# Kernel optimization log

Hardware: AMD Instinct MI355X
Metric: run time of the kernel (lower is better)

The kernel has to match this reference:

```python
import jax, jax.numpy as jnp
import numpy as np

SIGMA = 0.1
CAPACITY_FACTOR = 1.25


def setup_inputs() -> dict:
    key = jax.random.key(0)
    ks = jax.random.split(key, 5)
    B, T, D, E, H = 4, 2048, 1024, 16, 4096
    x = jax.random.normal(ks[0], (B, T, D), dtype=jnp.float32)
    token_mask = jnp.ones((B, T), dtype=bool)
    noise = jax.random.uniform(ks[1], (B * T, E), dtype=jnp.float32)
    W_router = jax.random.normal(ks[2], (D, E), dtype=jnp.float32) * 0.02
    W1 = jax.random.normal(ks[3], (E, D, H), dtype=jnp.float32) * 0.02
    W2 = jax.random.normal(ks[4], (E, H, D), dtype=jnp.float32) * 0.02
    return {"x": x, "token_mask": token_mask, "noise": noise,
            "W_router": W_router, "W1": W1, "W2": W2}


def reference(x, token_mask, noise, W_router, W1, W2):
    B, T, D = x.shape
    E = W_router.shape[1]
    N = B * T
    cap = int(N * CAPACITY_FACTOR / E)  # static capacity (mask is full)

    xf = x.reshape(N, D)
    mask = token_mask.reshape(N)

    # --- router (noisy gating) ---
    logits_clean = xf @ W_router                           # [N, E]
    mult = 1.0 + (noise * 2.0 - 1.0) * SIGMA
    mult = jnp.where(mask[:, None], mult, 1.0)
    logits = logits_clean * mult
    probs = jax.nn.softmax(logits, axis=-1)
    eid = jnp.argmax(probs, axis=-1)                       # [N]
    gate = jnp.take_along_axis(probs, eid[:, None], axis=1)[:, 0]

    probs_clean = jax.nn.softmax(logits_clean, axis=-1)
    eid_clean = jnp.argmax(probs_clean, axis=-1)

    # --- aux losses (over masked tokens) ---
    n_all = jnp.sum(mask).astype(logits_clean.dtype)
    p = jnp.sum(jnp.where(mask[:, None], probs_clean, 0.0), axis=0) / n_all
    f = jnp.sum(jnp.where(mask[:, None], jax.nn.one_hot(eid_clean, E, dtype=logits_clean.dtype), 0.0), axis=0) / n_all
    lb_loss = E * jnp.sum(p * f)
    z = jax.nn.logsumexp(logits_clean, axis=-1)
    z_loss = jnp.sum(jnp.where(mask, z * z, 0.0)) / n_all

    # --- capacity dispatch: per expert keep top-cap tokens by gate ---
    eid_eff = jnp.where(mask, eid, E)                      # masked tokens -> sentinel E
    order = jnp.lexsort((-gate, eid_eff))                  # by expert asc, gate desc
    sorted_e = eid_eff[order]
    pos = jnp.arange(N) - jnp.searchsorted(sorted_e, sorted_e, side="left")
    keep = (pos < cap) & (sorted_e < E)                    # dispatch mask (sorted)
    slot = jnp.where(keep, sorted_e * cap + pos, E * cap)  # overflow row for dropped

    buf = jnp.zeros((E * cap + 1, D), dtype=x.dtype)
    buf = buf.at[slot].set(jnp.where(keep[:, None], xf[order], 0.0))
    buf_e = buf[: E * cap].reshape(E, cap, D)

    # --- per-expert FFN, output scaled by gate ---
    h = jax.nn.relu(jnp.einsum("ecd,edh->ech", buf_e, W1))
    yb = jnp.einsum("ech,ehd->ecd", h, W2).reshape(E * cap, D)

    # --- combine: gather back, zero for dropped/masked tokens ---
    y_sorted = jnp.where(keep[:, None],
                         yb[jnp.clip(slot, 0, E * cap - 1)] * gate[order][:, None],
                         0.0)
    y = jnp.zeros((N, D), dtype=x.dtype).at[order].set(y_sorted)
    return y.reshape(B, T, D), lb_loss, z_loss
```

## Files before the change

### kernel.cpp

```cpp
#include <hip/hip_runtime.h>
#include <math.h>

#define N_TOK 8192
#define DMODEL 1024
#define NEXP 16
#define HDIM 4096
#define CAP 640
#define MYB 5
#define RANK_TPB 16
#define TP_RPAD 260

typedef __attribute__((ext_vector_type(8))) short bf16x8;
typedef __attribute__((ext_vector_type(4))) float f32x4;

#define OFF_EID   0
#define OFF_GATE  32768
#define OFF_SLOT  65536
#define OFF_PSUM  98304
#define OFF_Z2    (98304 + 64)
#define OFF_FCNT  (98304 + 128)
#define OFF_CNT   (98304 + 192)
#define OFF_BUF   131072
#define OFF_H     (OFF_BUF + 20971520)
#define OFF_WT    (OFF_H + 83886080)

__device__ inline unsigned short f2b(float f) {
    unsigned u = __builtin_bit_cast(unsigned, f);
    return (unsigned short)((u + 0x7fffu + ((u >> 16) & 1u)) >> 16);
}
__device__ inline float b2f(unsigned short b) {
    return __builtin_bit_cast(float, ((unsigned)b) << 16);
}

#define GLOAD_LDS16(g, l) __builtin_amdgcn_global_load_lds( \
    (__attribute__((address_space(1))) const void*)(g),      \
    (__attribute__((address_space(3))) void*)(l), 16, 0, 0)

__global__ __launch_bounds__(256) void router_kernel(
    const float* __restrict__ x, const float* __restrict__ noise,
    const float* __restrict__ Wr,
    int* __restrict__ eid, float* __restrict__ gate,
    float* __restrict__ p_sum, float* __restrict__ z2_sum,
    int* __restrict__ f_cnt, int* __restrict__ cnt_noisy)
{
    __shared__ float Wlds[1024 * 17];
    __shared__ float p_blk[16];
    __shared__ float z2_blk;
    int tid = threadIdx.x;
    for (int i = tid; i < 16384; i += 256) {
        int d = i >> 4, e = i & 15;
        Wlds[d * 17 + e] = Wr[i];
    }
    if (tid < 16) p_blk[tid] = 0.f;
    if (tid == 16) z2_blk = 0.f;
    __syncthreads();

    int lane = tid & 63;
    int wave = tid >> 6;

    for (int tt = 0; tt < 4; ++tt) {
        int t = blockIdx.x * 16 + wave * 4 + tt;
        const float* xr = x + (size_t)t * DMODEL;

        float acc[16];
#pragma unroll
        for (int e = 0; e < 16; ++e) acc[e] = 0.f;
        for (int c = 0; c < 16; ++c) {
            int d = c * 64 + lane;
            float xv = xr[d];
#pragma unroll
            for (int e = 0; e < 16; ++e)
                acc[e] = fmaf(xv, Wlds[d * 17 + e], acc[e]);
        }
#pragma unroll
        for (int e = 0; e < 16; ++e) {
#pragma unroll
            for (int m = 32; m >= 1; m >>= 1)
                acc[e] += __shfl_xor(acc[e], m, 64);
        }

        if (lane == 0) {
            float mx = acc[0]; int am = 0;
#pragma unroll
            for (int e = 1; e < 16; ++e) if (acc[e] > mx) { mx = acc[e]; am = e; }
            float pc[16]; float s = 0.f;
#pragma unroll
            for (int e = 0; e < 16; ++e) { pc[e] = expf(acc[e] - mx); s += pc[e]; }
            float inv = 1.f / s;
            float z = mx + logf(s);

            float ln[16];
#pragma unroll
            for (int e = 0; e < 16; ++e) {
                float nz = noise[(size_t)t * 16 + e];
                ln[e] = acc[e] * (1.f + (nz * 2.f - 1.f) * 0.1f);
            }
            float mxn = ln[0]; int amn = 0;
#pragma unroll
            for (int e = 1; e < 16; ++e) if (ln[e] > mxn) { mxn = ln[e]; amn = e; }
            float sn = 0.f;
#pragma unroll
            for (int e = 0; e < 16; ++e) sn += expf(ln[e] - mxn);
            float g = 1.f / sn;

            eid[t] = amn;
            gate[t] = g;
            atomicAdd(&f_cnt[am], 1);
            atomicAdd(&cnt_noisy[amn], 1);
#pragma unroll
            for (int e = 0; e < 16; ++e) atomicAdd(&p_blk[e], pc[e] * inv);
            atomicAdd(&z2_blk, z * z);
        }
    }
    __syncthreads();
    if (tid < 16) atomicAdd(&p_sum[tid], p_blk[tid]);
    if (tid == 16) atomicAdd(z2_sum, z2_blk);
}

__global__ __launch_bounds__(256) void rank_kernel(
    const int* __restrict__ eid, const float* __restrict__ gate,
    int* __restrict__ slot)
{
    __shared__ int   se[N_TOK];
    __shared__ float sg[N_TOK];
    int tid = threadIdx.x;
    for (int k = tid; k < N_TOK; k += 256) {
        se[k] = eid[k];
        sg[k] = gate[k];
    }
    __syncthreads();

    int wave = tid >> 6, lane = tid & 63;
    int base = blockIdx.x * RANK_TPB + wave * 4;

    int   my_e[4];
    float my_g[4];
    int   r[4] = {0, 0, 0, 0};
#pragma unroll
    for (int t = 0; t < 4; ++t) {
        my_e[t] = se[base + t];
        my_g[t] = sg[base + t];
    }

    for (int k = 0; k < N_TOK / 64; ++k) {
        int j = k * 64 + lane;
        int   ej = se[j];
        float gj = sg[j];
#pragma unroll
        for (int t = 0; t < 4; ++t) {
            int i = base + t;
            if (ej == my_e[t] && (gj > my_g[t] || (gj == my_g[t] && j < i))) r[t]++;
        }
    }
#pragma unroll
    for (int t = 0; t < 4; ++t) {
#pragma unroll
        for (int m = 32; m >= 1; m >>= 1)
            r[t] += __shfl_xor(r[t], m, 64);
    }
    if (lane < 4) {
        int t = lane;
        int rr = r[t];
        slot[base + t] = (rr < CAP) ? my_e[t] * CAP + rr : -1;
    }
}

__global__ __launch_bounds__(256) void scatter_kernel(
    const float* __restrict__ x, const int* __restrict__ slot,
    unsigned short* __restrict__ buf)
{
    int i = blockIdx.x;
    int s = slot[i];
    if (s < 0) return;
    float4 v = ((const float4*)(x + (size_t)i * DMODEL))[threadIdx.x];
    ushort4 o;
    o.x = f2b(v.x); o.y = f2b(v.y); o.z = f2b(v.z); o.w = f2b(v.w);
    ((ushort4*)(buf + (size_t)s * DMODEL))[threadIdx.x] = o;
}

__global__ __launch_bounds__(256) void transpose_cvt(
    const float* __restrict__ in, unsigned short* __restrict__ out,
    int R, int C)
{
    __shared__ unsigned short S[64][TP_RPAD];
    int e = blockIdx.z;
    const float* I = in + (size_t)e * R * C;
    unsigned short* O = out + (size_t)e * R * C;
    int r0 = blockIdx.y * 256, c0 = blockIdx.x * 64;
    int tid = threadIdx.x;

    int rr = tid >> 4;
    int c4 = (tid & 15) * 4;
#pragma unroll
    for (int s = 0; s < 16; ++s) {
        int row = s * 16 + rr;
        float4 v = *(const float4*)(I + (size_t)(r0 + row) * C + c0 + c4);
        S[c4 + 0][row] = f2b(v.x);
        S[c4 + 1][row] = f2b(v.y);
        S[c4 + 2][row] = f2b(v.z);
        S[c4 + 3][row] = f2b(v.w);
    }
    __syncthreads();

    int k4 = (tid & 63) * 4;
    int cb = tid >> 6;
#pragma unroll
    for (int u = 0; u < 16; ++u) {
        int c = cb + u * 4;
        ushort4 w = *(const ushort4*)&S[c][k4];
        *(ushort4*)(O + (size_t)(c0 + c) * R + r0 + k4) = w;
    }
}

template<int RELU>
__global__ __launch_bounds__(256) void gemm_mfma(
    const unsigned short* __restrict__ A,
    const unsigned short* __restrict__ BT,
    unsigned short* __restrict__ C,
    const int* __restrict__ cnt,
    int K, int N, int NX)
{
    unsigned orig = blockIdx.x;
    unsigned chunk = gridDim.x >> 3;
    unsigned logical = (orig & 7u) * chunk + (orig >> 3);
    unsigned my = logical % MYB;
    unsigned rest = logical / MYB;
    unsigned nx = rest % (unsigned)NX;
    unsigned e = rest / (unsigned)NX;

    int eff = cnt[e]; eff = eff < CAP ? eff : CAP;
    int m0 = my * 128;
    if (m0 >= eff) return;
    int n0 = nx * 128;
    const unsigned short* Ae  = A  + (size_t)e * CAP * K + (size_t)m0 * K;
    const unsigned short* BTe = BT + (size_t)e * N * K   + (size_t)n0 * K;
    unsigned short* Ce = C + (size_t)e * CAP * N;

    __shared__ unsigned short Asm[128 * 64];
    __shared__ unsigned short Bsm[128 * 64];

    int tid = threadIdx.x;
    int w = tid >> 6, lane = tid & 63;
    int l16 = lane & 15, quad = lane >> 4;
    int wy = w >> 1, wx = w & 1;

    f32x4 acc[4][4] = {};

    for (int k0 = 0; k0 < K; k0 += 64) {
#pragma unroll
        for (int i = 0; i < 4; ++i) {
            int s = i * 256 + w * 64 + lane;
            int r = s >> 3;
            int l = (s & 7) ^ (r & 7);
            const unsigned short* ga = Ae  + (size_t)r * K + k0 + l * 8;
            const unsigned short* gb = BTe + (size_t)r * K + k0 + l * 8;
            GLOAD_LDS16(ga, Asm + (i * 256 + w * 64) * 8);
            GLOAD_LDS16(gb, Bsm + (i * 256 + w * 64) * 8);
        }
        __syncthreads();
#pragma unroll
        for (int kk = 0; kk < 64; kk += 32) {
            bf16x8 af[4], bfr[4];
            int lc = (kk >> 3) + quad;
#pragma unroll
            for (int i = 0; i < 4; ++i) {
                int m = wy * 64 + i * 16 + l16;
                af[i] = *(const bf16x8*)(Asm + ((size_t)m * 8 + (lc ^ (m & 7))) * 8);
                int n = wx * 64 + i * 16 + l16;
                bfr[i] = *(const bf16x8*)(Bsm + ((size_t)n * 8 + (lc ^ (n & 7))) * 8);
            }
#pragma unroll
            for (int i = 0; i < 4; ++i)
#pragma unroll
                for (int j = 0; j < 4; ++j)
                    acc[i][j] = __builtin_amdgcn_mfma_f32_16x16x32_bf16(
                        af[i], bfr[j], acc[i][j], 0, 0, 0);
        }
        __syncthreads();
    }

#pragma unroll
    for (int i = 0; i < 4; ++i) {
        int rloc = wy * 64 + i * 16 + quad * 4;
        unsigned short* Cs = (wy == 0) ? Asm : Bsm;
        int rbase = rloc & 63;
#pragma unroll
        for (int j = 0; j < 4; ++j) {
            int cloc = wx * 64 + j * 16 + l16;
#pragma unroll
            for (int r = 0; r < 4; ++r) {
                float v = acc[i][j][r];
                if (RELU) v = fmaxf(v, 0.f);
                Cs[(rbase + r) * 128 + cloc] = f2b(v);
            }
        }
    }
    __syncthreads();
    {
        int rr2 = tid >> 4;
        int cc2 = (tid & 15) * 8;
#pragma unroll
        for (int p = 0; p < 8; ++p) {
            int rloc = p * 16 + rr2;
            const unsigned short* Cs = (p < 4) ? Asm : Bsm;
            int rbase = rloc & 63;
            bf16x8 v = *(const bf16x8*)(Cs + rbase * 128 + cc2);
            *(bf16x8*)(Ce + (size_t)(m0 + rloc) * N + n0 + cc2) = v;
        }
    }
}

__global__ __launch_bounds__(256) void combine_kernel(
    const unsigned short* __restrict__ yb, const int* __restrict__ slot,
    const float* __restrict__ gate, float* __restrict__ y,
    const float* __restrict__ p_sum, const float* __restrict__ z2,
    const int* __restrict__ f_cnt, float* __restrict__ loss_out)
{
    int i = blockIdx.x;
    int s = slot[i];
    float4 v = make_float4(0.f, 0.f, 0.f, 0.f);
    if (s >= 0) {
        float g = gate[i];
        ushort4 t = ((const ushort4*)(yb + (size_t)s * DMODEL))[threadIdx.x];
        v = make_float4(b2f(t.x) * g, b2f(t.y) * g, b2f(t.z) * g, b2f(t.w) * g);
    }
    ((float4*)(y + (size_t)i * DMODEL))[threadIdx.x] = v;

    if (i == 0 && threadIdx.x == 0) {
        float lb = 0.f;
        for (int e = 0; e < 16; ++e)
            lb += (p_sum[e] / 8192.f) * ((float)f_cnt[e] / 8192.f);
        loss_out[0] = 16.f * lb;
        loss_out[1] = z2[0] / 8192.f;
    }
}

extern "C" void kernel_launch(void* const* d_in, const int* in_sizes, int n_in,
                              void* d_out, int out_size, void* d_ws, size_t ws_size,
                              hipStream_t stream) {
    const float* x     = (const float*)d_in[0];
    const float* noise = (const float*)d_in[2];
    const float* Wr    = (const float*)d_in[3];
    const float* W1    = (const float*)d_in[4];
    const float* W2    = (const float*)d_in[5];
    float* out = (float*)d_out;

    char* ws = (char*)d_ws;
    int*   eid   = (int*)(ws + OFF_EID);
    float* gate  = (float*)(ws + OFF_GATE);
    int*   slot  = (int*)(ws + OFF_SLOT);
    float* p_sum = (float*)(ws + OFF_PSUM);
    float* z2    = (float*)(ws + OFF_Z2);
    int*   f_cnt = (int*)(ws + OFF_FCNT);
    int*   cnt   = (int*)(ws + OFF_CNT);
    unsigned short* buf = (unsigned short*)(ws + OFF_BUF);
    unsigned short* h   = (unsigned short*)(ws + OFF_H);
    unsigned short* wt  = (unsigned short*)(ws + OFF_WT);
    unsigned short* yb  = buf;

    hipMemsetAsync(ws + OFF_PSUM, 0, 256, stream);

    router_kernel<<<N_TOK / 16, 256, 0, stream>>>(x, noise, Wr, eid, gate,
                                                  p_sum, z2, f_cnt, cnt);
    rank_kernel<<<N_TOK / RANK_TPB, 256, 0, stream>>>(eid, gate, slot);
    scatter_kernel<<<N_TOK, 256, 0, stream>>>(x, slot, buf);

    transpose_cvt<<<dim3(HDIM / 64, DMODEL / 256, NEXP), 256, 0, stream>>>(
        W1, wt, DMODEL, HDIM);
    gemm_mfma<1><<<NEXP * (HDIM / 128) * MYB, 256, 0, stream>>>(
        buf, wt, h, cnt, DMODEL, HDIM, HDIM / 128);

    transpose_cvt<<<dim3(DMODEL / 64, HDIM / 256, NEXP), 256, 0, stream>>>(
        W2, wt, HDIM, DMODEL);
    gemm_mfma<0><<<NEXP * (DMODEL / 128) * MYB, 256, 0, stream>>>(
        h, wt, yb, cnt, HDIM, DMODEL, DMODEL / 128);

    combine_kernel<<<N_TOK, 256, 0, stream>>>(yb, slot, gate, out,
                                              p_sum, z2, f_cnt,
                                              out + (size_t)N_TOK * DMODEL);
}
```

Baseline: 978.5 us.

## Fuse rank and scatter kernels, aggregate router counts in LDS, hoist GEMM addresses

The rank kernel now writes each token's slot and copies its row, converted to bf16, into the expert buffer itself, so the separate scatter kernel launch and the slot re-read go away. The router accumulates per-block expert counts in shared memory and issues one global atomic per expert per block instead of one per token. The GEMM precomputes its per-lane global load pointers outside the k loop. Each wave in the fused kernel now copies 4 rows, which is less parallelism for the copy than the old one-block-per-token scatter.

```diff
diff --git a/kernel.cpp b/kernel.cpp
--- a/kernel.cpp
+++ b/kernel.cpp
@@ -45,13 +45,15 @@
 {
     __shared__ float Wlds[1024 * 17];
     __shared__ float p_blk[16];
+    __shared__ int   f_blk[16];
+    __shared__ int   c_blk[16];
     __shared__ float z2_blk;
     int tid = threadIdx.x;
     for (int i = tid; i < 16384; i += 256) {
         int d = i >> 4, e = i & 15;
         Wlds[d * 17 + e] = Wr[i];
     }
-    if (tid < 16) p_blk[tid] = 0.f;
+    if (tid < 16) { p_blk[tid] = 0.f; f_blk[tid] = 0; c_blk[tid] = 0; }
     if (tid == 16) z2_blk = 0.f;
     __syncthreads();
 
@@ -105,21 +107,26 @@
 
             eid[t] = amn;
             gate[t] = g;
-            atomicAdd(&f_cnt[am], 1);
-            atomicAdd(&cnt_noisy[amn], 1);
+            atomicAdd(&f_blk[am], 1);
+            atomicAdd(&c_blk[amn], 1);
 #pragma unroll
             for (int e = 0; e < 16; ++e) atomicAdd(&p_blk[e], pc[e] * inv);
             atomicAdd(&z2_blk, z * z);
         }
     }
     __syncthreads();
-    if (tid < 16) atomicAdd(&p_sum[tid], p_blk[tid]);
+    if (tid < 16) {
+        atomicAdd(&p_sum[tid], p_blk[tid]);
+        atomicAdd(&f_cnt[tid], f_blk[tid]);
+        atomicAdd(&cnt_noisy[tid], c_blk[tid]);
+    }
     if (tid == 16) atomicAdd(z2_sum, z2_blk);
 }
 
-__global__ __launch_bounds__(256) void rank_kernel(
+__global__ __launch_bounds__(256) void rank_scatter_kernel(
     const int* __restrict__ eid, const float* __restrict__ gate,
-    int* __restrict__ slot)
+    const float* __restrict__ x,
+    int* __restrict__ slot, unsigned short* __restrict__ buf)
 {
     __shared__ int   se[N_TOK];
     __shared__ float sg[N_TOK];
@@ -158,24 +165,31 @@
         for (int m = 32; m >= 1; m >>= 1)
             r[t] += __shfl_xor(r[t], m, 64);
     }
-    if (lane < 4) {
-        int t = lane;
-        int rr = r[t];
-        slot[base + t] = (rr < CAP) ? my_e[t] * CAP + rr : -1;
-    }
-}
-
-__global__ __launch_bounds__(256) void scatter_kernel(
-    const float* __restrict__ x, const int* __restrict__ slot,
-    unsigned short* __restrict__ buf)
-{
-    int i = blockIdx.x;
-    int s = slot[i];
-    if (s < 0) return;
-    float4 v = ((const float4*)(x + (size_t)i * DMODEL))[threadIdx.x];
-    ushort4 o;
-    o.x = f2b(v.x); o.y = f2b(v.y); o.z = f2b(v.z); o.w = f2b(v.w);
-    ((ushort4*)(buf + (size_t)s * DMODEL))[threadIdx.x] = o;
+
+    int sv[4];
+#pragma unroll
+    for (int t = 0; t < 4; ++t)
+        sv[t] = (r[t] < CAP) ? my_e[t] * CAP + r[t] : -1;
+#pragma unroll
+    for (int t = 0; t < 4; ++t)
+        if (lane == t) slot[base + t] = sv[t];
+
+    const float4* x4 = (const float4*)x;
+    ushort4* b4 = (ushort4*)buf;
+#pragma unroll
+    for (int t = 0; t < 4; ++t) {
+        int s = sv[t];
+        if (s < 0) continue;
+        size_t iro = (size_t)(base + t) * 256;
+        size_t oro = (size_t)s * 256;
+#pragma unroll
+        for (int q = 0; q < 4; ++q) {
+            float4 v = x4[iro + q * 64 + lane];
+            ushort4 o;
+            o.x = f2b(v.x); o.y = f2b(v.y); o.z = f2b(v.z); o.w = f2b(v.w);
+            b4[oro + q * 64 + lane] = o;
+        }
+    }
 }
 
 __global__ __launch_bounds__(256) void transpose_cvt(
@@ -244,18 +258,24 @@
     int l16 = lane & 15, quad = lane >> 4;
     int wy = w >> 1, wx = w & 1;
 
+    const unsigned short* pa[4];
+    const unsigned short* pb[4];
+#pragma unroll
+    for (int i = 0; i < 4; ++i) {
+        int s = i * 256 + w * 64 + lane;
+        int r = s >> 3;
+        int l = (s & 7) ^ (r & 7);
+        pa[i] = Ae  + (size_t)r * K + l * 8;
+        pb[i] = BTe + (size_t)r * K + l * 8;
+    }
+
     f32x4 acc[4][4] = {};
 
     for (int k0 = 0; k0 < K; k0 += 64) {
 #pragma unroll
         for (int i = 0; i < 4; ++i) {
-            int s = i * 256 + w * 64 + lane;
-            int r = s >> 3;
-            int l = (s & 7) ^ (r & 7);
-            const unsigned short* ga = Ae  + (size_t)r * K + k0 + l * 8;
-            const unsigned short* gb = BTe + (size_t)r * K + k0 + l * 8;
-            GLOAD_LDS16(ga, Asm + (i * 256 + w * 64) * 8);
-            GLOAD_LDS16(gb, Bsm + (i * 256 + w * 64) * 8);
+            GLOAD_LDS16(pa[i] + k0, Asm + (i * 256 + w * 64) * 8);
+            GLOAD_LDS16(pb[i] + k0, Bsm + (i * 256 + w * 64) * 8);
         }
         __syncthreads();
 #pragma unroll
@@ -362,8 +382,8 @@
 
     router_kernel<<<N_TOK / 16, 256, 0, stream>>>(x, noise, Wr, eid, gate,
                                                   p_sum, z2, f_cnt, cnt);
-    rank_kernel<<<N_TOK / RANK_TPB, 256, 0, stream>>>(eid, gate, slot);
-    scatter_kernel<<<N_TOK, 256, 0, stream>>>(x, slot, buf);
+    rank_scatter_kernel<<<N_TOK / RANK_TPB, 256, 0, stream>>>(eid, gate, x,
+                                                              slot, buf);
 
     transpose_cvt<<<dim3(HDIM / 64, DMODEL / 256, NEXP), 256, 0, stream>>>(
         W1, wt, DMODEL, HDIM);
```

New measurement: 922.6 us. -5.7%, faster.
